# Kernel optimization log

Hardware: AMD Instinct MI355X
Metric: run time of the kernel (lower is better)

## Reference

```python
import jax, jax.numpy as jnp
import numpy as np

N = 16      # num_nodes
D = 128     # embedding_dim
H = 8       # num_heads
F = 512     # feedforward_dim
L = 4       # num_layers
IN = 64     # per-node input dim (joint_pos 32 + joint_vel 32)
B = 16384   # batch


def _ln(x, g, b):
    m = x.mean(-1, keepdims=True)
    v = ((x - m) ** 2).mean(-1, keepdims=True)
    return (x - m) * jax.lax.rsqrt(v + 1e-5) * g + b


def setup_inputs() -> dict:
    key = jax.random.key(0)
    ks = jax.random.split(key, 24)
    s = 0.02
    inp = {
        'joint_pos': jax.random.normal(ks[0], (B, 32), jnp.float32),
        'joint_vel': jax.random.normal(ks[1], (B, 32), jnp.float32),
        'adjacency': jax.random.randint(ks[2], (N, N), 0, 2).astype(jnp.int32),
        # per-node embedder (distinct Linear per node, stacked)
        'embed_W': jax.random.normal(ks[3], (N, IN, D), jnp.float32) * s,
        'embed_b': jnp.zeros((N, D), jnp.float32),
        'pos_emb': jax.random.normal(ks[4], (N, D), jnp.float32) * s,
        # per-layer attention params, stacked over layer dim
        'Wq': jax.random.normal(ks[5], (L, D, D), jnp.float32) * s,
        'bq': jnp.zeros((L, D), jnp.float32),
        'Wk': jax.random.normal(ks[6], (L, D, D), jnp.float32) * s,
        'bk': jnp.zeros((L, D), jnp.float32),
        'Wv': jax.random.normal(ks[7], (L, D, D), jnp.float32) * s,
        'bv': jnp.zeros((L, D), jnp.float32),
        'Wo': jax.random.normal(ks[8], (L, D, D), jnp.float32) * s,
        'bo': jnp.zeros((L, D), jnp.float32),
        'ln1_g': jnp.ones((L, D), jnp.float32),
        'ln1_b': jnp.zeros((L, D), jnp.float32),
        'ln2_g': jnp.ones((L, D), jnp.float32),
        'ln2_b': jnp.zeros((L, D), jnp.float32),
        'W1': jax.random.normal(ks[9], (L, D, F), jnp.float32) * s,
        'b1': jnp.zeros((L, F), jnp.float32),
        'W2': jax.random.normal(ks[10], (L, F, D), jnp.float32) * s,
        'b2': jnp.zeros((L, D), jnp.float32),
    }
    return inp


def reference(joint_pos, joint_vel, adjacency, embed_W, embed_b, pos_emb,
              Wq, bq, Wk, bk, Wv, bv, Wo, bo,
              ln1_g, ln1_b, ln2_g, ln2_b, W1, b1, W2, b2):
    # adjacency with forced self-loops -> additive attention mask [N, N]
    adj = adjacency.astype(bool) | jnp.eye(N, dtype=bool)
    mask = jnp.where(adj, 0.0, -jnp.inf).astype(jnp.float32)

    # every node sees the full concatenated obs (list-variant obs_node_dict)
    feats = jnp.concatenate([joint_pos, joint_vel], axis=-1)        # [B, IN]
    # distinct per-node linear embedders, batched as one einsum
    x = jnp.einsum('bi,nio->bno', feats, embed_W) + embed_b + pos_emb  # [B, N, D]

    dh = D // H
    scale = 1.0 / (dh ** 0.5)
    for l in range(L):  # BoT-Hard: mask on every layer; pre-LN
        h = _ln(x, ln1_g[l], ln1_b[l])
        q = (h @ Wq[l] + bq[l]).reshape(-1, N, H, dh)
        k = (h @ Wk[l] + bk[l]).reshape(-1, N, H, dh)
        v = (h @ Wv[l] + bv[l]).reshape(-1, N, H, dh)
        s = jnp.einsum('bnhd,bmhd->bhnm', q, k) * scale + mask       # [B, H, N, N]
        a = jax.nn.softmax(s, axis=-1)
        o = jnp.einsum('bhnm,bmhd->bnhd', a, v).reshape(-1, N, D)
        x = x + o @ Wo[l] + bo[l]
        h2 = _ln(x, ln2_g[l], ln2_b[l])
        x = x + jax.nn.relu(h2 @ W1[l] + b1[l]) @ W2[l] + b2[l]
    return x
```

## Files before the change

kernel.cpp:

```cpp
#include <hip/hip_runtime.h>
#include <stdint.h>

typedef __bf16 bf16;
typedef bf16 bf16x8 __attribute__((ext_vector_type(8)));
typedef bf16 bf16x4 __attribute__((ext_vector_type(4)));
typedef float f32x4 __attribute__((ext_vector_type(4)));
typedef uint32_t u32;
typedef uint8_t u8;

#define B_TOT 16384
#define SWG 8
#define NWGS (B_TOT / SWG)

__device__ __forceinline__ f32x4 mfma32(bf16x8 a, bf16x8 b, f32x4 c) {
  return __builtin_amdgcn_mfma_f32_16x16x32_bf16(a, b, c, 0, 0, 0);
}
__device__ __forceinline__ bf16x8 zero8() {
  bf16x8 v;
#pragma unroll
  for (int j = 0; j < 8; j++) v[j] = (bf16)0.f;
  return v;
}

__device__ __forceinline__ void bar_lg() {
  __builtin_amdgcn_sched_barrier(0);
  asm volatile("s_waitcnt lgkmcnt(0)" ::: "memory");
  __builtin_amdgcn_s_barrier();
  __builtin_amdgcn_sched_barrier(0);
}
__device__ __forceinline__ void bar_v0() {
  __builtin_amdgcn_sched_barrier(0);
  asm volatile("s_waitcnt vmcnt(0) lgkmcnt(0)" ::: "memory");
  __builtin_amdgcn_s_barrier();
  __builtin_amdgcn_sched_barrier(0);
}

__device__ __forceinline__ void stage32(const u8* __restrict__ src, int rowstride, int colbase,
                                        u8* dst, int tid) {
  __builtin_amdgcn_sched_barrier(0);
#pragma unroll
  for (int rr = 0; rr < 4; ++rr) {
    u32 o = (u32)(rr * 512 + tid) * 16u;
    u32 row = o >> 8, cb = o & 0xF0u;
    const u8* s = src + (size_t)row * (size_t)rowstride + (size_t)colbase
                      + (size_t)(cb ^ ((row & 7u) << 4));
    __builtin_amdgcn_global_load_lds((const __attribute__((address_space(1))) u32*)s,
                                     (__attribute__((address_space(3))) u32*)(dst + o),
                                     16, 0, 0);
  }
  __builtin_amdgcn_sched_barrier(0);
}

__device__ __forceinline__ bf16x8 wread32(const u8* Wb, int row, u32 koff) {
  return *(const bf16x8*)(Wb + (u32)(row * 256) + (koff ^ (((u32)row & 7u) << 4)));
}

__device__ __forceinline__ void st_row(u8* base, int row, int col, bf16 v) {
  *(bf16*)(base + (u32)(row * 256) + (u32)((2 * col) ^ ((row & 15) << 4))) = v;
}

__device__ __forceinline__ void loadA_rm(const u8* R, int g, int c, bf16x8 a[2][4]) {
  const u32 sw = (u32)c << 4;
#pragma unroll
  for (int mt = 0; mt < 2; ++mt)
#pragma unroll
    for (int ks = 0; ks < 4; ++ks)
      a[mt][ks] = *(const bf16x8*)(R + (u32)((mt * 16 + c) * 256)
                                     + (((u32)(ks * 64 + g * 16)) ^ sw));
}

__device__ __forceinline__ void gemm_full(const u8* Wb, const bf16x8 a[2][4],
                                          f32x4 acc[2][4], int nh, int g, int c) {
#pragma unroll
  for (int ks = 0; ks < 4; ++ks)
#pragma unroll
    for (int nt = 0; nt < 4; ++nt) {
      bf16x8 b = wread32(Wb, nh * 64 + nt * 16 + c, (u32)(ks * 64 + g * 16));
      acc[0][nt] = mfma32(a[0][ks], b, acc[0][nt]);
      acc[1][nt] = mfma32(a[1][ks], b, acc[1][nt]);
    }
}

template <bool RELU>
__device__ __forceinline__ void epi_rm(const f32x4 acc[2][4], const float* __restrict__ bias,
                                       u8* Rdst, int nh, int g, int c) {
#pragma unroll
  for (int nt = 0; nt < 4; ++nt) {
    int col = nh * 64 + nt * 16 + c;
    float bb = bias[col];
#pragma unroll
    for (int mt = 0; mt < 2; ++mt)
#pragma unroll
      for (int r = 0; r < 4; ++r) {
        float v = acc[mt][nt][r] + bb;
        if (RELU) v = fmaxf(v, 0.f);
        st_row(Rdst, mt * 16 + 4 * g + r, col, (bf16)v);
      }
  }
}

__device__ __forceinline__ void pack4(const f32x4 v, u32& w0, u32& w1) {
  union { bf16 h[2]; u32 u; } t0, t1;
  t0.h[0] = (bf16)v[0]; t0.h[1] = (bf16)v[1];
  t1.h[0] = (bf16)v[2]; t1.h[1] = (bf16)v[3];
  w0 = t0.u; w1 = t1.u;
}

__device__ __forceinline__ bf16x8 Rfrag(u32 w0, u32 w1, int g, int c) {
  int s0 = 32 * g + c;
  int s1 = 32 * g + 16 + c;
  u32 a0 = (u32)__shfl((int)w0, s0);
  u32 a1 = (u32)__shfl((int)w1, s0);
  u32 a2 = (u32)__shfl((int)w0, s1);
  u32 a3 = (u32)__shfl((int)w1, s1);
  union { u32 u[4]; bf16x8 v; } r;
  bool ok = (g < 2);
  r.u[0] = ok ? a0 : 0u; r.u[1] = ok ? a1 : 0u;
  r.u[2] = ok ? a2 : 0u; r.u[3] = ok ? a3 : 0u;
  return r.v;
}

__device__ __forceinline__ void ln_part(const f32x4 x[2][4], float sS[2][4], float sS2[2][4]) {
#pragma unroll
  for (int mt = 0; mt < 2; ++mt) {
    f32x4 a = {0.f, 0.f, 0.f, 0.f}, b = {0.f, 0.f, 0.f, 0.f};
#pragma unroll
    for (int nt = 0; nt < 4; ++nt) { a += x[mt][nt]; b += x[mt][nt] * x[mt][nt]; }
#pragma unroll
    for (int r = 0; r < 4; ++r) {
      float s = a[r], s2 = b[r];
#pragma unroll
      for (int off = 1; off < 16; off <<= 1) { s += __shfl_xor(s, off); s2 += __shfl_xor(s2, off); }
      sS[mt][r] = s; sS2[mt][r] = s2;
    }
  }
}

__global__ void __launch_bounds__(512, 2)
bot_main(const int* __restrict__ adj,
         const float* __restrict__ embB, const float* __restrict__ posE,
         const float* __restrict__ pbq, const float* __restrict__ pbk,
         const float* __restrict__ pbv, const float* __restrict__ pbo,
         const float* __restrict__ l1g, const float* __restrict__ l1b,
         const float* __restrict__ l2g, const float* __restrict__ l2b,
         const float* __restrict__ pb1, const float* __restrict__ pb2,
         const bf16* __restrict__ feats, const bf16* __restrict__ embWT,
         const bf16* __restrict__ wqT, const bf16* __restrict__ wkT,
         const bf16* __restrict__ wvT, const bf16* __restrict__ woT,
         const bf16* __restrict__ w1T, const bf16* __restrict__ w2T,
         float* __restrict__ out) {
  __shared__ u8 smem[163840];
  const int tid = threadIdx.x;
  const int w = tid >> 6, lane = tid & 63, g = lane >> 4, c = lane & 15;
  const int p = w >> 1, nh = w & 1;
  const int S0 = blockIdx.x * SWG;

  u8* pairb = smem + p * 24576;
  u8* Th = pairb;
  u8* Tq = pairb + 8192;
  u8* Tk = pairb + 16384;
  u8* WA = smem + 98304;
  u8* WB = smem + 131072;
  float* scr = (float*)Tk;

  float maskT[4];
#pragma unroll
  for (int r = 0; r < 4; ++r) {
    int m = 4 * g + r;
    maskT[r] = (adj[c * 16 + m] != 0 || c == m) ? 0.f : -1e9f;
  }

  {
    float* x0 = (float*)smem;
    bf16x8 af[2];
#pragma unroll
    for (int ks = 0; ks < 2; ++ks)
      af[ks] = *(const bf16x8*)(feats + (size_t)(S0 + (c & 7)) * 64 + ks * 32 + g * 8);
    f32x4 ea[16] = {};
#pragma unroll
    for (int nt = 0; nt < 16; ++nt)
#pragma unroll
      for (int ks = 0; ks < 2; ++ks) {
        bf16x8 bw = *(const bf16x8*)(embWT + (size_t)(w * 256 + nt * 16 + c) * 64 + ks * 32 + g * 8);
        ea[nt] = mfma32(af[ks], bw, ea[nt]);
      }
    if (g < 2) {
#pragma unroll
      for (int nt = 0; nt < 16; ++nt)
#pragma unroll
        for (int r = 0; r < 4; ++r)
          x0[(4 * g + r) * 2048 + w * 256 + nt * 16 + c] = ea[nt][r];
    }
  }
  __syncthreads();

  f32x4 x[2][4];
  {
    const float* x0 = (const float*)smem;
#pragma unroll
    for (int nt = 0; nt < 4; ++nt)
#pragma unroll
      for (int r = 0; r < 4; ++r) {
        int n = 4 * g + r, d = nh * 64 + nt * 16 + c;
        float eb = embB[n * 128 + d] + posE[n * 128 + d];
#pragma unroll
        for (int mt = 0; mt < 2; ++mt)
          x[mt][nt][r] = x0[(2 * p + mt) * 2048 + n * 128 + d] + eb;
      }
  }
  __syncthreads();

  bf16x8 Ah[2][4], Ah2[2][4], Au[2][4];

#pragma unroll 1
  for (int l = 0; l < 4; ++l) {
    const u8* Wq_l = (const u8*)(wqT + (size_t)l * 16384);
    const u8* Wk_l = (const u8*)(wkT + (size_t)l * 16384);
    const u8* Wv_l = (const u8*)(wvT + (size_t)l * 16384);
    const u8* Wo_l = (const u8*)(woT + (size_t)l * 16384);
    const u8* W1_l = (const u8*)(w1T + (size_t)l * 65536);
    const u8* W2_l = (const u8*)(w2T + (size_t)l * 65536);

    float sS[2][4], sS2[2][4], mean[2][4], rstd[2][4];
    const f32x4 zz = {0.f, 0.f, 0.f, 0.f};

    ln_part(x, sS, sS2);
    if (c == 0) {
#pragma unroll
      for (int mt = 0; mt < 2; ++mt)
#pragma unroll
        for (int r = 0; r < 4; ++r) {
          int row = mt * 16 + 4 * g + r;
          scr[(row * 2 + nh) * 2 + 0] = sS[mt][r];
          scr[(row * 2 + nh) * 2 + 1] = sS2[mt][r];
        }
    }
    bar_lg();

    stage32(Wq_l, 256, 0, WA, tid);
#pragma unroll
    for (int mt = 0; mt < 2; ++mt)
#pragma unroll
      for (int r = 0; r < 4; ++r) {
        int row = mt * 16 + 4 * g + r;
        float s = sS[mt][r] + scr[(row * 2 + (1 - nh)) * 2 + 0];
        float s2 = sS2[mt][r] + scr[(row * 2 + (1 - nh)) * 2 + 1];
        float mu = s * (1.f / 128.f);
        float va = s2 * (1.f / 128.f) - mu * mu;
        mean[mt][r] = mu; rstd[mt][r] = rsqrtf(va + 1e-5f);
      }
#pragma unroll
    for (int nt = 0; nt < 4; ++nt) {
      int col = nh * 64 + nt * 16 + c;
      float gg = l1g[l * 128 + col], bb = l1b[l * 128 + col];
#pragma unroll
      for (int mt = 0; mt < 2; ++mt)
#pragma unroll
        for (int r = 0; r < 4; ++r)
          st_row(Th, mt * 16 + 4 * g + r, col,
                 (bf16)((x[mt][nt][r] - mean[mt][r]) * rstd[mt][r] * gg + bb));
    }
    bar_v0();

    f32x4 acc[2][4];
    stage32(Wk_l, 256, 0, WB, tid);
    loadA_rm(Th, g, c, Ah);
#pragma unroll
    for (int mt = 0; mt < 2; ++mt)
#pragma unroll
      for (int nt = 0; nt < 4; ++nt) acc[mt][nt] = zz;
    gemm_full(WA, Ah, acc, nh, g, c);
    epi_rm<false>(acc, pbq + l * 128, Tq, nh, g, c);
    bar_v0();

    stage32(Wv_l, 256, 0, WA, tid);
#pragma unroll
    for (int mt = 0; mt < 2; ++mt)
#pragma unroll
      for (int nt = 0; nt < 4; ++nt) acc[mt][nt] = zz;
    gemm_full(WB, Ah, acc, nh, g, c);
    epi_rm<false>(acc, pbk + l * 128, Tk, nh, g, c);
    bar_v0();

    stage32(Wo_l, 256, 0, WB, tid);
    {
      bf16x8 Vf[2][4];
#pragma unroll
      for (int mt = 0; mt < 2; ++mt)
#pragma unroll
        for (int nt = 0; nt < 4; ++nt) acc[mt][nt] = zz;
      gemm_full(WA, Ah, acc, nh, g, c);
#pragma unroll
      for (int nt = 0; nt < 4; ++nt) {
        float bb = pbv[l * 128 + nh * 64 + nt * 16 + c];
#pragma unroll
        for (int mt = 0; mt < 2; ++mt) {
          f32x4 v;
#pragma unroll
          for (int r = 0; r < 4; ++r) v[r] = acc[mt][nt][r] + bb;
          u32 w0, w1; pack4(v, w0, w1);
          Vf[mt][nt] = Rfrag(w0, w1, g, c);
        }
      }
      const u32 swa = (u32)c << 4;
#pragma unroll
      for (int hh = 0; hh < 4; ++hh) {
        const int gh = nh * 4 + hh;
        bf16x8 qf[2], kf[2];
#pragma unroll
        for (int mt = 0; mt < 2; ++mt) {
          if (g < 2) {
            qf[mt] = *(const bf16x8*)(Tq + (u32)((mt * 16 + c) * 256)
                                         + (((u32)(gh * 32 + g * 16)) ^ swa));
            kf[mt] = *(const bf16x8*)(Tk + (u32)((mt * 16 + c) * 256)
                                         + (((u32)(gh * 32 + g * 16)) ^ swa));
          } else { qf[mt] = zero8(); kf[mt] = zero8(); }
        }
#pragma unroll
        for (int mt = 0; mt < 2; ++mt) {
          f32x4 st = mfma32(kf[mt], qf[mt], zz);
          float pr[4];
#pragma unroll
          for (int r = 0; r < 4; ++r) pr[r] = st[r] * 0.25f + maskT[r];
          float mx = fmaxf(fmaxf(pr[0], pr[1]), fmaxf(pr[2], pr[3]));
          mx = fmaxf(mx, __shfl_xor(mx, 16));
          mx = fmaxf(mx, __shfl_xor(mx, 32));
          float sm = 0.f;
#pragma unroll
          for (int r = 0; r < 4; ++r) { pr[r] = __expf(pr[r] - mx); sm += pr[r]; }
          sm += __shfl_xor(sm, 16);
          sm += __shfl_xor(sm, 32);
          float pinv = __fdividef(1.f, sm);
          f32x4 pv;
#pragma unroll
          for (int r = 0; r < 4; ++r) pv[r] = pr[r] * pinv;
          u32 w0, w1; pack4(pv, w0, w1);
          bf16x8 Pf = Rfrag(w0, w1, g, c);
          f32x4 oo = mfma32(Vf[mt][hh], Pf, zz);
          pack4(oo, w0, w1);
          bf16x8 Of = Rfrag(w0, w1, g, c);
          if (g < 2)
            *(bf16x8*)(Tq + (u32)((mt * 16 + c) * 256)
                          + (((u32)(gh * 32 + g * 16)) ^ swa)) = Of;
        }
      }
    }
    bar_v0();

    loadA_rm(Tq, g, c, Ah);
    gemm_full(WB, Ah, x, nh, g, c);
#pragma unroll
    for (int nt = 0; nt < 4; ++nt) {
      float bb = pbo[l * 128 + nh * 64 + nt * 16 + c];
#pragma unroll
      for (int mt = 0; mt < 2; ++mt)
#pragma unroll
        for (int r = 0; r < 4; ++r) x[mt][nt][r] += bb;
    }
    ln_part(x, sS, sS2);
    if (c == 0) {
#pragma unroll
      for (int mt = 0; mt < 2; ++mt)
#pragma unroll
        for (int r = 0; r < 4; ++r) {
          int row = mt * 16 + 4 * g + r;
          scr[(row * 2 + nh) * 2 + 0] = sS[mt][r];
          scr[(row * 2 + nh) * 2 + 1] = sS2[mt][r];
        }
    }
    bar_lg();

    stage32(W1_l, 256, 0, WA, tid);
#pragma unroll
    for (int mt = 0; mt < 2; ++mt)
#pragma unroll
      for (int r = 0; r < 4; ++r) {
        int row = mt * 16 + 4 * g + r;
        float s = sS[mt][r] + scr[(row * 2 + (1 - nh)) * 2 + 0];
        float s2 = sS2[mt][r] + scr[(row * 2 + (1 - nh)) * 2 + 1];
        float mu = s * (1.f / 128.f);
        float va = s2 * (1.f / 128.f) - mu * mu;
        mean[mt][r] = mu; rstd[mt][r] = rsqrtf(va + 1e-5f);
      }
#pragma unroll
    for (int nt = 0; nt < 4; ++nt) {
      int col = nh * 64 + nt * 16 + c;
      float gg = l2g[l * 128 + col], bb = l2b[l * 128 + col];
#pragma unroll
      for (int mt = 0; mt < 2; ++mt)
#pragma unroll
        for (int r = 0; r < 4; ++r)
          st_row(Th, mt * 16 + 4 * g + r, col,
                 (bf16)((x[mt][nt][r] - mean[mt][r]) * rstd[mt][r] * gg + bb));
    }
    bar_v0();

#pragma unroll 1
    for (int fc = 0; fc < 4; ++fc) {
      stage32(W2_l, 1024, fc * 256, WB, tid);
      if (fc == 0) loadA_rm(Th, g, c, Ah2);
      f32x4 uacc[2][4];
#pragma unroll
      for (int mt = 0; mt < 2; ++mt)
#pragma unroll
        for (int nt = 0; nt < 4; ++nt) uacc[mt][nt] = zz;
      gemm_full(WA, Ah2, uacc, nh, g, c);
      epi_rm<true>(uacc, pb1 + l * 512 + fc * 128, Tq, nh, g, c);
      bar_v0();
      if (fc < 3) stage32(W1_l + (fc + 1) * 32768, 256, 0, WA, tid);
      loadA_rm(Tq, g, c, Au);
      gemm_full(WB, Au, x, nh, g, c);
      if (fc < 3) bar_v0();
      else {
#pragma unroll
        for (int nt = 0; nt < 4; ++nt) {
          float bb = pb2[l * 128 + nh * 64 + nt * 16 + c];
#pragma unroll
          for (int mt = 0; mt < 2; ++mt)
#pragma unroll
            for (int r = 0; r < 4; ++r) x[mt][nt][r] += bb;
        }
        bar_lg();
      }
    }
  }

#pragma unroll
  for (int nt = 0; nt < 4; ++nt) {
    int col = nh * 64 + nt * 16 + c;
#pragma unroll
    for (int mt = 0; mt < 2; ++mt)
      *(f32x4*)(pairb + mt * 8192 + col * 64 + g * 16) = x[mt][nt];
  }
  bar_lg();
  {
    const int smp = S0 + 2 * p + nh;
    const u8* src = pairb + nh * 8192;
#pragma unroll
    for (int it = 0; it < 8; ++it) {
      int n = it * 2 + (lane >> 5);
      int slot = lane & 31;
      f32x4 v;
#pragma unroll
      for (int e = 0; e < 4; ++e)
        v[e] = *(const float*)(src + (u32)((slot * 4 + e) * 64 + n * 4));
      __builtin_nontemporal_store(v, (f32x4*)(out + (size_t)smp * 2048 + n * 128 + slot * 4));
    }
  }
}

__global__ void prep_feats_k(const float* __restrict__ pos, const float* __restrict__ vel,
                             bf16* __restrict__ feats) {
  int i = blockIdx.x * 256 + threadIdx.x;
  if (i >= B_TOT * 64) return;
  int b = i >> 6, k = i & 63;
  float v = (k < 32) ? pos[b * 32 + k] : vel[b * 32 + (k - 32)];
  feats[i] = (bf16)v;
}

__global__ void prep_tr_k(const float* __restrict__ src, bf16* __restrict__ dst,
                          int R, int C, int total) {
  int i = blockIdx.x * 256 + threadIdx.x;
  if (i >= total) return;
  int rc = R * C;
  int m = i / rc, rem = i % rc;
  int cc = rem / R, rr = rem % R;
  dst[i] = (bf16)src[(size_t)m * rc + rr * C + cc];
}

extern "C" void kernel_launch(void* const* d_in, const int* in_sizes, int n_in,
                              void* d_out, int out_size, void* d_ws, size_t ws_size,
                              hipStream_t stream) {
  const float* jp  = (const float*)d_in[0];
  const float* jv  = (const float*)d_in[1];
  const int*   adj = (const int*)d_in[2];
  const float* eW  = (const float*)d_in[3];
  const float* eB  = (const float*)d_in[4];
  const float* pE  = (const float*)d_in[5];
  const float* Wq  = (const float*)d_in[6];  const float* bq = (const float*)d_in[7];
  const float* Wk  = (const float*)d_in[8];  const float* bk = (const float*)d_in[9];
  const float* Wv  = (const float*)d_in[10]; const float* bv = (const float*)d_in[11];
  const float* Wo  = (const float*)d_in[12]; const float* bo = (const float*)d_in[13];
  const float* g1  = (const float*)d_in[14]; const float* be1 = (const float*)d_in[15];
  const float* g2  = (const float*)d_in[16]; const float* be2 = (const float*)d_in[17];
  const float* W1  = (const float*)d_in[18]; const float* b1 = (const float*)d_in[19];
  const float* W2  = (const float*)d_in[20]; const float* b2 = (const float*)d_in[21];

  bf16* ws    = (bf16*)d_ws;
  bf16* feats = ws;
  bf16* embWT = ws + 1048576;
  bf16* wqT   = embWT + 131072;
  bf16* wkT   = wqT + 65536;
  bf16* wvT   = wkT + 65536;
  bf16* woT   = wvT + 65536;
  bf16* w1T   = woT + 65536;
  bf16* w2T   = w1T + 262144;

  prep_feats_k<<<(B_TOT * 64 + 255) / 256, 256, 0, stream>>>(jp, jv, feats);
  prep_tr_k<<<512, 256, 0, stream>>>(eW, embWT, 64, 128, 131072);
  prep_tr_k<<<256, 256, 0, stream>>>(Wq, wqT, 128, 128, 65536);
  prep_tr_k<<<256, 256, 0, stream>>>(Wk, wkT, 128, 128, 65536);
  prep_tr_k<<<256, 256, 0, stream>>>(Wv, wvT, 128, 128, 65536);
  prep_tr_k<<<256, 256, 0, stream>>>(Wo, woT, 128, 128, 65536);
  prep_tr_k<<<1024, 256, 0, stream>>>(W1, w1T, 128, 512, 262144);
  prep_tr_k<<<1024, 256, 0, stream>>>(W2, w2T, 512, 128, 262144);

  bot_main<<<NWGS, 512, 0, stream>>>(adj, eB, pE, bq, bk, bv, bo,
                                     g1, be1, g2, be2, b1, b2,
                                     feats, embWT, wqT, wkT, wvT, woT, w1T, w2T,
                                     (float*)d_out);
}
```

Before: 1.036 ms.

## Regroup warps into quads of four samples with 32-column output slices

Warps are now grouped four per block of four samples (64 rows), each owning a 32-column slice, where before they were paired per two samples with 64-column halves. Each B fragment read from LDS is reused across four M tiles instead of two, and A fragments are loaded per k-step inside the GEMM rather than held in registers across GEMMs. This cuts LDS weight reads per MFMA and lowers register pressure from the cached A fragments. In exchange, activation reads from LDS increase, LayerNorm partial sums now combine four slices through scratch, and the per-group LDS buffers are larger.

```diff
diff --git a/kernel.cpp b/kernel.cpp
--- a/kernel.cpp
+++ b/kernel.cpp
@@ -59,42 +59,40 @@
   *(bf16*)(base + (u32)(row * 256) + (u32)((2 * col) ^ ((row & 15) << 4))) = v;
 }
 
-__device__ __forceinline__ void loadA_rm(const u8* R, int g, int c, bf16x8 a[2][4]) {
-  const u32 sw = (u32)c << 4;
-#pragma unroll
-  for (int mt = 0; mt < 2; ++mt)
-#pragma unroll
-    for (int ks = 0; ks < 4; ++ks)
-      a[mt][ks] = *(const bf16x8*)(R + (u32)((mt * 16 + c) * 256)
-                                     + (((u32)(ks * 64 + g * 16)) ^ sw));
-}
-
-__device__ __forceinline__ void gemm_full(const u8* Wb, const bf16x8 a[2][4],
-                                          f32x4 acc[2][4], int nh, int g, int c) {
-#pragma unroll
-  for (int ks = 0; ks < 4; ++ks)
-#pragma unroll
-    for (int nt = 0; nt < 4; ++nt) {
-      bf16x8 b = wread32(Wb, nh * 64 + nt * 16 + c, (u32)(ks * 64 + g * 16));
-      acc[0][nt] = mfma32(a[0][ks], b, acc[0][nt]);
-      acc[1][nt] = mfma32(a[1][ks], b, acc[1][nt]);
-    }
+__device__ __forceinline__ void gemm_q(const u8* Wb, const u8* Ta, f32x4 acc[4][2],
+                                       int qn, int g, int c) {
+  const u32 swA = (u32)c << 4;
+#pragma unroll
+  for (int ks = 0; ks < 4; ++ks) {
+    bf16x8 a[4];
+#pragma unroll
+    for (int s = 0; s < 4; ++s)
+      a[s] = *(const bf16x8*)(Ta + (u32)((s * 16 + c) * 256)
+                                 + (((u32)(ks * 64 + g * 16)) ^ swA));
+#pragma unroll
+    for (int nt = 0; nt < 2; ++nt) {
+      bf16x8 b = wread32(Wb, qn * 32 + nt * 16 + c, (u32)(ks * 64 + g * 16));
+#pragma unroll
+      for (int s = 0; s < 4; ++s)
+        acc[s][nt] = mfma32(a[s], b, acc[s][nt]);
+    }
+  }
 }
 
 template <bool RELU>
-__device__ __forceinline__ void epi_rm(const f32x4 acc[2][4], const float* __restrict__ bias,
-                                       u8* Rdst, int nh, int g, int c) {
-#pragma unroll
-  for (int nt = 0; nt < 4; ++nt) {
-    int col = nh * 64 + nt * 16 + c;
+__device__ __forceinline__ void epi_q(const f32x4 acc[4][2], const float* __restrict__ bias,
+                                      u8* Rdst, int qn, int g, int c) {
+#pragma unroll
+  for (int nt = 0; nt < 2; ++nt) {
+    int col = qn * 32 + nt * 16 + c;
     float bb = bias[col];
 #pragma unroll
-    for (int mt = 0; mt < 2; ++mt)
+    for (int s = 0; s < 4; ++s)
 #pragma unroll
       for (int r = 0; r < 4; ++r) {
-        float v = acc[mt][nt][r] + bb;
+        float v = acc[s][nt][r] + bb;
         if (RELU) v = fmaxf(v, 0.f);
-        st_row(Rdst, mt * 16 + 4 * g + r, col, (bf16)v);
+        st_row(Rdst, s * 16 + 4 * g + r, col, (bf16)v);
       }
   }
 }
@@ -120,18 +118,17 @@
   return r.v;
 }
 
-__device__ __forceinline__ void ln_part(const f32x4 x[2][4], float sS[2][4], float sS2[2][4]) {
-#pragma unroll
-  for (int mt = 0; mt < 2; ++mt) {
-    f32x4 a = {0.f, 0.f, 0.f, 0.f}, b = {0.f, 0.f, 0.f, 0.f};
-#pragma unroll
-    for (int nt = 0; nt < 4; ++nt) { a += x[mt][nt]; b += x[mt][nt] * x[mt][nt]; }
+__device__ __forceinline__ void ln_part4(const f32x4 x[4][2], float sS[4][4], float sS2[4][4]) {
+#pragma unroll
+  for (int s = 0; s < 4; ++s) {
+    f32x4 a = x[s][0] + x[s][1];
+    f32x4 b = x[s][0] * x[s][0] + x[s][1] * x[s][1];
 #pragma unroll
     for (int r = 0; r < 4; ++r) {
-      float s = a[r], s2 = b[r];
-#pragma unroll
-      for (int off = 1; off < 16; off <<= 1) { s += __shfl_xor(s, off); s2 += __shfl_xor(s2, off); }
-      sS[mt][r] = s; sS2[mt][r] = s2;
+      float u = a[r], u2 = b[r];
+#pragma unroll
+      for (int off = 1; off < 16; off <<= 1) { u += __shfl_xor(u, off); u2 += __shfl_xor(u2, off); }
+      sS[s][r] = u; sS2[s][r] = u2;
     }
   }
 }
@@ -152,13 +149,13 @@
   __shared__ u8 smem[163840];
   const int tid = threadIdx.x;
   const int w = tid >> 6, lane = tid & 63, g = lane >> 4, c = lane & 15;
-  const int p = w >> 1, nh = w & 1;
+  const int p = w >> 2, qn = w & 3;
   const int S0 = blockIdx.x * SWG;
 
-  u8* pairb = smem + p * 24576;
+  u8* pairb = smem + p * 49152;
   u8* Th = pairb;
-  u8* Tq = pairb + 8192;
-  u8* Tk = pairb + 16384;
+  u8* Tq = pairb + 16384;
+  u8* Tk = pairb + 32768;
   u8* WA = smem + 98304;
   u8* WB = smem + 131072;
   float* scr = (float*)Tk;
@@ -194,23 +191,21 @@
   }
   __syncthreads();
 
-  f32x4 x[2][4];
+  f32x4 x[4][2];
   {
     const float* x0 = (const float*)smem;
 #pragma unroll
-    for (int nt = 0; nt < 4; ++nt)
+    for (int nt = 0; nt < 2; ++nt)
 #pragma unroll
       for (int r = 0; r < 4; ++r) {
-        int n = 4 * g + r, d = nh * 64 + nt * 16 + c;
+        int n = 4 * g + r, d = qn * 32 + nt * 16 + c;
         float eb = embB[n * 128 + d] + posE[n * 128 + d];
 #pragma unroll
-        for (int mt = 0; mt < 2; ++mt)
-          x[mt][nt][r] = x0[(2 * p + mt) * 2048 + n * 128 + d] + eb;
+        for (int s = 0; s < 4; ++s)
+          x[s][nt][r] = x0[(4 * p + s) * 2048 + n * 128 + d] + eb;
       }
   }
   __syncthreads();
-
-  bf16x8 Ah[2][4], Ah2[2][4], Au[2][4];
 
 #pragma unroll 1
   for (int l = 0; l < 4; ++l) {
@@ -221,104 +216,104 @@
     const u8* W1_l = (const u8*)(w1T + (size_t)l * 65536);
     const u8* W2_l = (const u8*)(w2T + (size_t)l * 65536);
 
-    float sS[2][4], sS2[2][4], mean[2][4], rstd[2][4];
+    float sS[4][4], sS2[4][4], mean[4][4], rstd[4][4];
     const f32x4 zz = {0.f, 0.f, 0.f, 0.f};
 
-    ln_part(x, sS, sS2);
+    ln_part4(x, sS, sS2);
     if (c == 0) {
 #pragma unroll
-      for (int mt = 0; mt < 2; ++mt)
+      for (int s = 0; s < 4; ++s)
 #pragma unroll
         for (int r = 0; r < 4; ++r) {
-          int row = mt * 16 + 4 * g + r;
-          scr[(row * 2 + nh) * 2 + 0] = sS[mt][r];
-          scr[(row * 2 + nh) * 2 + 1] = sS2[mt][r];
+          int row = s * 16 + 4 * g + r;
+          scr[(row * 4 + qn) * 2 + 0] = sS[s][r];
+          scr[(row * 4 + qn) * 2 + 1] = sS2[s][r];
         }
     }
     bar_lg();
 
     stage32(Wq_l, 256, 0, WA, tid);
 #pragma unroll
-    for (int mt = 0; mt < 2; ++mt)
+    for (int s = 0; s < 4; ++s)
 #pragma unroll
       for (int r = 0; r < 4; ++r) {
-        int row = mt * 16 + 4 * g + r;
-        float s = sS[mt][r] + scr[(row * 2 + (1 - nh)) * 2 + 0];
-        float s2 = sS2[mt][r] + scr[(row * 2 + (1 - nh)) * 2 + 1];
-        float mu = s * (1.f / 128.f);
-        float va = s2 * (1.f / 128.f) - mu * mu;
-        mean[mt][r] = mu; rstd[mt][r] = rsqrtf(va + 1e-5f);
-      }
-#pragma unroll
-    for (int nt = 0; nt < 4; ++nt) {
-      int col = nh * 64 + nt * 16 + c;
+        int row = s * 16 + 4 * g + r;
+        float u = 0.f, u2 = 0.f;
+#pragma unroll
+        for (int qq = 0; qq < 4; ++qq) {
+          u += scr[(row * 4 + qq) * 2 + 0];
+          u2 += scr[(row * 4 + qq) * 2 + 1];
+        }
+        float mu = u * (1.f / 128.f);
+        float va = u2 * (1.f / 128.f) - mu * mu;
+        mean[s][r] = mu; rstd[s][r] = rsqrtf(va + 1e-5f);
+      }
+#pragma unroll
+    for (int nt = 0; nt < 2; ++nt) {
+      int col = qn * 32 + nt * 16 + c;
       float gg = l1g[l * 128 + col], bb = l1b[l * 128 + col];
 #pragma unroll
-      for (int mt = 0; mt < 2; ++mt)
+      for (int s = 0; s < 4; ++s)
 #pragma unroll
         for (int r = 0; r < 4; ++r)
-          st_row(Th, mt * 16 + 4 * g + r, col,
-                 (bf16)((x[mt][nt][r] - mean[mt][r]) * rstd[mt][r] * gg + bb));
+          st_row(Th, s * 16 + 4 * g + r, col,
+                 (bf16)((x[s][nt][r] - mean[s][r]) * rstd[s][r] * gg + bb));
     }
     bar_v0();
 
-    f32x4 acc[2][4];
+    f32x4 acc[4][2];
     stage32(Wk_l, 256, 0, WB, tid);
-    loadA_rm(Th, g, c, Ah);
-#pragma unroll
-    for (int mt = 0; mt < 2; ++mt)
-#pragma unroll
-      for (int nt = 0; nt < 4; ++nt) acc[mt][nt] = zz;
-    gemm_full(WA, Ah, acc, nh, g, c);
-    epi_rm<false>(acc, pbq + l * 128, Tq, nh, g, c);
+#pragma unroll
+    for (int s = 0; s < 4; ++s)
+#pragma unroll
+      for (int nt = 0; nt < 2; ++nt) acc[s][nt] = zz;
+    gemm_q(WA, Th, acc, qn, g, c);
+    epi_q<false>(acc, pbq + l * 128, Tq, qn, g, c);
     bar_v0();
 
     stage32(Wv_l, 256, 0, WA, tid);
 #pragma unroll
-    for (int mt = 0; mt < 2; ++mt)
-#pragma unroll
-      for (int nt = 0; nt < 4; ++nt) acc[mt][nt] = zz;
-    gemm_full(WB, Ah, acc, nh, g, c);
-    epi_rm<false>(acc, pbk + l * 128, Tk, nh, g, c);
+    for (int s = 0; s < 4; ++s)
+#pragma unroll
+      for (int nt = 0; nt < 2; ++nt) acc[s][nt] = zz;
+    gemm_q(WB, Th, acc, qn, g, c);
+    epi_q<false>(acc, pbk + l * 128, Tk, qn, g, c);
     bar_v0();
 
     stage32(Wo_l, 256, 0, WB, tid);
     {
-      bf16x8 Vf[2][4];
-#pragma unroll
-      for (int mt = 0; mt < 2; ++mt)
-#pragma unroll
-        for (int nt = 0; nt < 4; ++nt) acc[mt][nt] = zz;
-      gemm_full(WA, Ah, acc, nh, g, c);
-#pragma unroll
-      for (int nt = 0; nt < 4; ++nt) {
-        float bb = pbv[l * 128 + nh * 64 + nt * 16 + c];
-#pragma unroll
-        for (int mt = 0; mt < 2; ++mt) {
+      bf16x8 Vf[4][2];
+#pragma unroll
+      for (int s = 0; s < 4; ++s)
+#pragma unroll
+        for (int nt = 0; nt < 2; ++nt) acc[s][nt] = zz;
+      gemm_q(WA, Th, acc, qn, g, c);
+#pragma unroll
+      for (int nt = 0; nt < 2; ++nt) {
+        float bb = pbv[l * 128 + qn * 32 + nt * 16 + c];
+#pragma unroll
+        for (int s = 0; s < 4; ++s) {
           f32x4 v;
 #pragma unroll
-          for (int r = 0; r < 4; ++r) v[r] = acc[mt][nt][r] + bb;
+          for (int r = 0; r < 4; ++r) v[r] = acc[s][nt][r] + bb;
           u32 w0, w1; pack4(v, w0, w1);
-          Vf[mt][nt] = Rfrag(w0, w1, g, c);
+          Vf[s][nt] = Rfrag(w0, w1, g, c);
         }
       }
       const u32 swa = (u32)c << 4;
 #pragma unroll
-      for (int hh = 0; hh < 4; ++hh) {
-        const int gh = nh * 4 + hh;
-        bf16x8 qf[2], kf[2];
-#pragma unroll
-        for (int mt = 0; mt < 2; ++mt) {
+      for (int hh = 0; hh < 2; ++hh) {
+        const int gh = qn * 2 + hh;
+#pragma unroll
+        for (int s = 0; s < 4; ++s) {
+          bf16x8 qf, kf;
           if (g < 2) {
-            qf[mt] = *(const bf16x8*)(Tq + (u32)((mt * 16 + c) * 256)
-                                         + (((u32)(gh * 32 + g * 16)) ^ swa));
-            kf[mt] = *(const bf16x8*)(Tk + (u32)((mt * 16 + c) * 256)
-                                         + (((u32)(gh * 32 + g * 16)) ^ swa));
-          } else { qf[mt] = zero8(); kf[mt] = zero8(); }
-        }
-#pragma unroll
-        for (int mt = 0; mt < 2; ++mt) {
-          f32x4 st = mfma32(kf[mt], qf[mt], zz);
+            qf = *(const bf16x8*)(Tq + (u32)((s * 16 + c) * 256)
+                                     + (((u32)(gh * 32 + g * 16)) ^ swa));
+            kf = *(const bf16x8*)(Tk + (u32)((s * 16 + c) * 256)
+                                     + (((u32)(gh * 32 + g * 16)) ^ swa));
+          } else { qf = zero8(); kf = zero8(); }
+          f32x4 st = mfma32(kf, qf, zz);
           float pr[4];
 #pragma unroll
           for (int r = 0; r < 4; ++r) pr[r] = st[r] * 0.25f + maskT[r];
@@ -336,89 +331,90 @@
           for (int r = 0; r < 4; ++r) pv[r] = pr[r] * pinv;
           u32 w0, w1; pack4(pv, w0, w1);
           bf16x8 Pf = Rfrag(w0, w1, g, c);
-          f32x4 oo = mfma32(Vf[mt][hh], Pf, zz);
+          f32x4 oo = mfma32(Vf[s][hh], Pf, zz);
           pack4(oo, w0, w1);
           bf16x8 Of = Rfrag(w0, w1, g, c);
           if (g < 2)
-            *(bf16x8*)(Tq + (u32)((mt * 16 + c) * 256)
+            *(bf16x8*)(Tq + (u32)((s * 16 + c) * 256)
                           + (((u32)(gh * 32 + g * 16)) ^ swa)) = Of;
         }
       }
     }
     bar_v0();
 
-    loadA_rm(Tq, g, c, Ah);
-    gemm_full(WB, Ah, x, nh, g, c);
-#pragma unroll
-    for (int nt = 0; nt < 4; ++nt) {
-      float bb = pbo[l * 128 + nh * 64 + nt * 16 + c];
-#pragma unroll
-      for (int mt = 0; mt < 2; ++mt)
-#pragma unroll
-        for (int r = 0; r < 4; ++r) x[mt][nt][r] += bb;
-    }
-    ln_part(x, sS, sS2);
+    gemm_q(WB, Tq, x, qn, g, c);
+#pragma unroll
+    for (int nt = 0; nt < 2; ++nt) {
+      float bb = pbo[l * 128 + qn * 32 + nt * 16 + c];
+#pragma unroll
+      for (int s = 0; s < 4; ++s)
+#pragma unroll
+        for (int r = 0; r < 4; ++r) x[s][nt][r] += bb;
+    }
+    ln_part4(x, sS, sS2);
     if (c == 0) {
 #pragma unroll
-      for (int mt = 0; mt < 2; ++mt)
+      for (int s = 0; s < 4; ++s)
 #pragma unroll
         for (int r = 0; r < 4; ++r) {
-          int row = mt * 16 + 4 * g + r;
-          scr[(row * 2 + nh) * 2 + 0] = sS[mt][r];
-          scr[(row * 2 + nh) * 2 + 1] = sS2[mt][r];
+          int row = s * 16 + 4 * g + r;
+          scr[(row * 4 + qn) * 2 + 0] = sS[s][r];
+          scr[(row * 4 + qn) * 2 + 1] = sS2[s][r];
         }
     }
     bar_lg();
 
     stage32(W1_l, 256, 0, WA, tid);
 #pragma unroll
-    for (int mt = 0; mt < 2; ++mt)
+    for (int s = 0; s < 4; ++s)
 #pragma unroll
       for (int r = 0; r < 4; ++r) {
-        int row = mt * 16 + 4 * g + r;
-        float s = sS[mt][r] + scr[(row * 2 + (1 - nh)) * 2 + 0];
-        float s2 = sS2[mt][r] + scr[(row * 2 + (1 - nh)) * 2 + 1];
-        float mu = s * (1.f / 128.f);
-        float va = s2 * (1.f / 128.f) - mu * mu;
-        mean[mt][r] = mu; rstd[mt][r] = rsqrtf(va + 1e-5f);
-      }
-#pragma unroll
-    for (int nt = 0; nt < 4; ++nt) {
-      int col = nh * 64 + nt * 16 + c;
+        int row = s * 16 + 4 * g + r;
+        float u = 0.f, u2 = 0.f;
+#pragma unroll
+        for (int qq = 0; qq < 4; ++qq) {
+          u += scr[(row * 4 + qq) * 2 + 0];
+          u2 += scr[(row * 4 + qq) * 2 + 1];
+        }
+        float mu = u * (1.f / 128.f);
+        float va = u2 * (1.f / 128.f) - mu * mu;
+        mean[s][r] = mu; rstd[s][r] = rsqrtf(va + 1e-5f);
+      }
+#pragma unroll
+    for (int nt = 0; nt < 2; ++nt) {
+      int col = qn * 32 + nt * 16 + c;
       float gg = l2g[l * 128 + col], bb = l2b[l * 128 + col];
 #pragma unroll
-      for (int mt = 0; mt < 2; ++mt)
+      for (int s = 0; s < 4; ++s)
 #pragma unroll
         for (int r = 0; r < 4; ++r)
-          st_row(Th, mt * 16 + 4 * g + r, col,
-                 (bf16)((x[mt][nt][r] - mean[mt][r]) * rstd[mt][r] * gg + bb));
+          st_row(Th, s * 16 + 4 * g + r, col,
+                 (bf16)((x[s][nt][r] - mean[s][r]) * rstd[s][r] * gg + bb));
     }
     bar_v0();
 
 #pragma unroll 1
     for (int fc = 0; fc < 4; ++fc) {
       stage32(W2_l, 1024, fc * 256, WB, tid);
-      if (fc == 0) loadA_rm(Th, g, c, Ah2);
-      f32x4 uacc[2][4];
-#pragma unroll
-      for (int mt = 0; mt < 2; ++mt)
-#pragma unroll
-        for (int nt = 0; nt < 4; ++nt) uacc[mt][nt] = zz;
-      gemm_full(WA, Ah2, uacc, nh, g, c);
-      epi_rm<true>(uacc, pb1 + l * 512 + fc * 128, Tq, nh, g, c);
+      f32x4 uacc[4][2];
+#pragma unroll
+      for (int s = 0; s < 4; ++s)
+#pragma unroll
+        for (int nt = 0; nt < 2; ++nt) uacc[s][nt] = zz;
+      gemm_q(WA, Th, uacc, qn, g, c);
+      epi_q<true>(uacc, pb1 + l * 512 + fc * 128, Tq, qn, g, c);
       bar_v0();
       if (fc < 3) stage32(W1_l + (fc + 1) * 32768, 256, 0, WA, tid);
-      loadA_rm(Tq, g, c, Au);
-      gemm_full(WB, Au, x, nh, g, c);
+      gemm_q(WB, Tq, x, qn, g, c);
       if (fc < 3) bar_v0();
       else {
 #pragma unroll
-        for (int nt = 0; nt < 4; ++nt) {
-          float bb = pb2[l * 128 + nh * 64 + nt * 16 + c];
-#pragma unroll
-          for (int mt = 0; mt < 2; ++mt)
-#pragma unroll
-            for (int r = 0; r < 4; ++r) x[mt][nt][r] += bb;
+        for (int nt = 0; nt < 2; ++nt) {
+          float bb = pb2[l * 128 + qn * 32 + nt * 16 + c];
+#pragma unroll
+          for (int s = 0; s < 4; ++s)
+#pragma unroll
+            for (int r = 0; r < 4; ++r) x[s][nt][r] += bb;
         }
         bar_lg();
       }
@@ -426,16 +422,16 @@
   }
 
 #pragma unroll
-  for (int nt = 0; nt < 4; ++nt) {
-    int col = nh * 64 + nt * 16 + c;
-#pragma unroll
-    for (int mt = 0; mt < 2; ++mt)
-      *(f32x4*)(pairb + mt * 8192 + col * 64 + g * 16) = x[mt][nt];
+  for (int nt = 0; nt < 2; ++nt) {
+    int col = qn * 32 + nt * 16 + c;
+#pragma unroll
+    for (int s = 0; s < 4; ++s)
+      *(f32x4*)(smem + (4 * p + s) * 8192 + col * 64 + g * 16) = x[s][nt];
   }
   bar_lg();
   {
-    const int smp = S0 + 2 * p + nh;
-    const u8* src = pairb + nh * 8192;
+    const int smp = S0 + w;
+    const u8* src = smem + w * 8192;
 #pragma unroll
     for (int it = 0; it < 8; ++it) {
       int n = it * 2 + (lane >> 5);
```

New measurement: 1.060 ms. 1.02x slower.
